# Kernel tuning notes

Measured on AMD Instinct MI355X. Metric: run time of the kernel, lower is better.

Reference implementation:

```python
import jax, jax.numpy as jnp
import numpy as np

N = 50000
E = 800000
IN_C = 16
H = 64
EA = 3
L = 3
EPS = 1e-5

def layer_norm(h, g, b):
    mu = jnp.mean(h, axis=-1, keepdims=True)
    var = jnp.var(h, axis=-1, keepdims=True)
    return (h - mu) * jax.lax.rsqrt(var + EPS) * g + b

def setup_inputs() -> dict:
    key = jax.random.key(0)
    ks = jax.random.split(key, 24)
    s = lambda *sh: 0.05
    d = {}
    d["x"] = jax.random.normal(ks[0], (N, IN_C), jnp.float32)
    d["edge_index"] = jax.random.randint(ks[1], (2, E), 0, N, jnp.int32)
    d["edge_attr"] = jax.random.normal(ks[2], (E, EA), jnp.float32)
    # encoder
    d["enc_w"] = jax.random.normal(ks[3], (IN_C, H), jnp.float32) * 0.1
    d["enc_b"] = jnp.zeros((H,), jnp.float32)
    d["enc_ln_g"] = jnp.ones((H,), jnp.float32)
    d["enc_ln_b"] = jnp.zeros((H,), jnp.float32)
    # message-passing MLPs (stacked over layers)
    d["mlp_w1"] = jax.random.normal(ks[4], (L, H + EA, H // 2), jnp.float32) * 0.1
    d["mlp_b1"] = jnp.zeros((L, H // 2), jnp.float32)
    d["mlp_w2"] = jax.random.normal(ks[5], (L, H // 2, H), jnp.float32) * 0.1
    d["mlp_b2"] = jnp.zeros((L, H), jnp.float32)
    d["ln_g"] = jnp.ones((L, H), jnp.float32)
    d["ln_b"] = jnp.zeros((L, H), jnp.float32)
    # heads
    d["depth_w1"] = jax.random.normal(ks[6], (H, H // 2), jnp.float32) * 0.1
    d["depth_b1"] = jnp.zeros((H // 2,), jnp.float32)
    d["depth_w2"] = jax.random.normal(ks[7], (H // 2, 1), jnp.float32) * 0.1
    d["depth_b2"] = jnp.zeros((1,), jnp.float32)
    d["vel_w1"] = jax.random.normal(ks[8], (H, H // 2), jnp.float32) * 0.1
    d["vel_b1"] = jnp.zeros((H // 2,), jnp.float32)
    d["vel_w2"] = jax.random.normal(ks[9], (H // 2, 2), jnp.float32) * 0.1
    d["vel_b2"] = jnp.zeros((2,), jnp.float32)
    return d

def reference(x, edge_index, edge_attr, enc_w, enc_b, enc_ln_g, enc_ln_b,
              mlp_w1, mlp_b1, mlp_w2, mlp_b2, ln_g, ln_b,
              depth_w1, depth_b1, depth_w2, depth_b2,
              vel_w1, vel_b1, vel_w2, vel_b2):
    src, dst = edge_index[0], edge_index[1]  # PyG: x_j = x[src], aggregate at dst
    # encoder (dropout inactive in eval mode)
    h = layer_norm(x @ enc_w + enc_b, enc_ln_g, enc_ln_b)
    h = jax.nn.relu(h)
    # in-degree counts for mean aggregation (isolated nodes -> 0, like PyG)
    cnt = jax.ops.segment_sum(jnp.ones((E,), jnp.float32), dst, num_segments=N)
    inv_cnt = jnp.where(cnt > 0, 1.0 / jnp.maximum(cnt, 1.0), 0.0)[:, None]
    for i in range(L):
        m_in = jnp.concatenate([h[src], edge_attr], axis=1)          # [E, H+EA]
        m = jax.nn.relu(m_in @ mlp_w1[i] + mlp_b1[i]) @ mlp_w2[i] + mlp_b2[i]  # [E, H]
        agg = jax.ops.segment_sum(m, dst, num_segments=N) * inv_cnt  # mean aggregate
        h = layer_norm(h + agg, ln_g[i], ln_b[i])
    depth = jax.nn.relu(h @ depth_w1 + depth_b1) @ depth_w2 + depth_b2    # [N,1]
    velocity = jax.nn.relu(h @ vel_w1 + vel_b1) @ vel_w2 + vel_b2         # [N,2]
    return (depth, velocity)
```

## Files before the change

### kernel.cpp

```cpp
#include <hip/hip_runtime.h>
#include <hip/hip_bf16.h>
#include <hip/hip_fp16.h>

typedef __hip_bfloat16 bf16;
typedef unsigned int u32;
typedef unsigned int u2v __attribute__((ext_vector_type(2)));

#define NN 50000
#define NE 800000
#define INC 16
#define HD 64
#define EPSV 1e-5f
#define NB1 196
#define CNTB 3125
#define ENCB 12500

__device__ __forceinline__ float b2f(bf16 v) { return __bfloat162float(v); }
__device__ __forceinline__ bool is_bf(const void* det) {
  return *(const u32*)det == 0x3F803F80u;
}

__device__ __forceinline__ uint2 ldnt2(const uint2* p) {
  u2v t = __builtin_nontemporal_load(reinterpret_cast<const u2v*>(p));
  uint2 r; r.x = t[0]; r.y = t[1];
  return r;
}

template<typename T> __device__ __forceinline__ float ldv(const T* p, int i);
template<> __device__ __forceinline__ float ldv<float>(const float* p, int i) { return p[i]; }
template<> __device__ __forceinline__ float ldv<bf16>(const bf16* p, int i) { return b2f(p[i]); }

#define W1F   0
#define B1F   6432
#define W2F   6528
#define B2F   12672
#define DW1F  12864
#define DB1F  14912
#define DW2F  14944
#define DB2F  14976
#define VW1F  14977
#define VB1F  17025
#define VW2F  17057
#define VB2F  17121
#define WFTOT 17123

#define H_OFF    0
#define P0_OFF   3200000
#define CSR_OFF  4800000
#define WF_OFF   8000000
#define CNTI_OFF (WF_OFF + WFTOT)
#define RS_OFF   (CNTI_OFF + NN)
#define BSUM_OFF (RS_OFF + NN)
#define BOFF_OFF (BSUM_OFF + 256)
#define LPOS_OFF (BOFF_OFF + 256)
#define INV_OFF  (LPOS_OFF + NE)
#define P1_OFF   (INV_OFF + NE)
#define WS_NEED_ROOMY ((size_t)(P1_OFF + NN * 16) * 4)

template<typename T>
__device__ __forceinline__ void prep_body(
    const T* w1, const T* b1, const T* w2, const T* b2,
    const T* dw1, const T* db1, const T* dw2, const T* db2,
    const T* vw1, const T* vb1, const T* vw2, const T* vb2,
    float* wf, int i) {
  float v;
  if      (i < B1F)  v = ldv(w1,  i - W1F);
  else if (i < W2F)  v = ldv(b1,  i - B1F);
  else if (i < B2F)  v = ldv(w2,  i - W2F);
  else if (i < DW1F) v = ldv(b2,  i - B2F);
  else if (i < DB1F) v = ldv(dw1, i - DW1F);
  else if (i < DW2F) v = ldv(db1, i - DB1F);
  else if (i < DB2F) v = ldv(dw2, i - DW2F);
  else if (i < VW1F) v = ldv(db2, i - DB2F);
  else if (i < VB1F) v = ldv(vw1, i - VW1F);
  else if (i < VW2F) v = ldv(vb1, i - VB1F);
  else if (i < VB2F) v = ldv(vw2, i - VW2F);
  else               v = ldv(vb2, i - VB2F);
  wf[i] = v;
}

__global__ __launch_bounds__(256) void prep_kernel(
    const void* w1, const void* b1, const void* w2, const void* b2,
    const void* dw1, const void* db1, const void* dw2, const void* db2,
    const void* vw1, const void* vb1, const void* vw2, const void* vb2,
    float* __restrict__ wf, const void* __restrict__ det) {
  int i = blockIdx.x * blockDim.x + threadIdx.x;
  if (i >= WFTOT) return;
  if (is_bf(det))
    prep_body((const bf16*)w1, (const bf16*)b1, (const bf16*)w2, (const bf16*)b2,
              (const bf16*)dw1, (const bf16*)db1, (const bf16*)dw2, (const bf16*)db2,
              (const bf16*)vw1, (const bf16*)vb1, (const bf16*)vw2, (const bf16*)vb2, wf, i);
  else
    prep_body((const float*)w1, (const float*)b1, (const float*)w2, (const float*)b2,
              (const float*)dw1, (const float*)db1, (const float*)dw2, (const float*)db2,
              (const float*)vw1, (const float*)vb1, (const float*)vw2, (const float*)vb2, wf, i);
}

__global__ __launch_bounds__(256) void enc_count_kernel(
    const void* __restrict__ x, const void* __restrict__ enc_w,
    const void* __restrict__ enc_b, const void* __restrict__ g,
    const void* __restrict__ b, float* __restrict__ h,
    __half* __restrict__ pout, const float* __restrict__ nw1,
    const float* __restrict__ nb1, const int* __restrict__ ei,
    int* __restrict__ cnt, int* __restrict__ lpos,
    const void* __restrict__ det) {
  if (blockIdx.x < CNTB) {
    int e = blockIdx.x * 256 + threadIdx.x;
    if (e < NE) lpos[e] = atomicAdd(&cnt[ei[NE + e]], 1);
    return;
  }
  __shared__ float shv[4][64];
  int node = ((blockIdx.x - CNTB) * blockDim.x + threadIdx.x) >> 6;
  int lane = threadIdx.x & 63;
  int w = threadIdx.x >> 6;
  if (node >= NN) return;
  int jl = lane & 31, half = lane >> 5;
  float xv[INC], wv[INC], ebv, gv, bv;
  if (is_bf(det)) {
    const bf16* xp = (const bf16*)x + node * INC;
    const bf16* wp = (const bf16*)enc_w;
    #pragma unroll
    for (int k = 0; k < INC; k++) { xv[k] = b2f(xp[k]); wv[k] = b2f(wp[k * HD + lane]); }
    ebv = b2f(((const bf16*)enc_b)[lane]);
    gv  = b2f(((const bf16*)g)[lane]);
    bv  = b2f(((const bf16*)b)[lane]);
  } else {
    const float* xp = (const float*)x + node * INC;
    const float* wp = (const float*)enc_w;
    #pragma unroll
    for (int k = 0; k < INC; k++) { xv[k] = xp[k]; wv[k] = wp[k * HD + lane]; }
    ebv = ((const float*)enc_b)[lane];
    gv  = ((const float*)g)[lane];
    bv  = ((const float*)b)[lane];
  }
  float acc = ebv;
  #pragma unroll
  for (int k = 0; k < INC; k++) acc += xv[k] * wv[k];
  float s1 = acc, s2 = acc * acc;
  #pragma unroll
  for (int o = 32; o; o >>= 1) { s1 += __shfl_xor(s1, o); s2 += __shfl_xor(s2, o); }
  float mu = s1 * (1.0f / 64.0f);
  float var = fmaxf(s2 * (1.0f / 64.0f) - mu * mu, 0.0f);
  float d = acc - mu;
  float hv = fmaxf(d * rsqrtf(var + EPSV) * gv + bv, 0.0f);
  h[node * HD + lane] = hv;
  shv[w][lane] = hv;
  float pacc = 0.0f;
  int kb = half << 5;
  #pragma unroll
  for (int k4 = 0; k4 < 32; k4 += 4) {
    float4 h4 = *reinterpret_cast<const float4*>(&shv[w][kb + k4]);
    int kk = kb + k4;
    pacc += h4.x * nw1[kk * 32 + jl] + h4.y * nw1[(kk + 1) * 32 + jl]
          + h4.z * nw1[(kk + 2) * 32 + jl] + h4.w * nw1[(kk + 3) * 32 + jl];
  }
  pacc += __shfl_xor(pacc, 32);
  if (half == 0) pout[node * 32 + jl] = __float2half(pacc + nb1[jl]);
}

__global__ __launch_bounds__(256) void scan1_kernel(const int* __restrict__ cnt,
                                                    int* __restrict__ ex,
                                                    int* __restrict__ bsum) {
  __shared__ int s[256];
  int t = threadIdx.x, idx = blockIdx.x * 256 + t;
  int v = (idx < NN) ? cnt[idx] : 0;
  s[t] = v;
  __syncthreads();
  #pragma unroll
  for (int off = 1; off < 256; off <<= 1) {
    int u = (t >= off) ? s[t - off] : 0;
    __syncthreads();
    s[t] += u;
    __syncthreads();
  }
  if (idx < NN) ex[idx] = s[t] - v;
  if (t == 255) bsum[blockIdx.x] = s[255];
}

__global__ __launch_bounds__(256) void scan2_kernel(int* __restrict__ bsum,
                                                    int* __restrict__ boff) {
  __shared__ int s[256];
  int t = threadIdx.x;
  int v = (t < NB1) ? bsum[t] : 0;
  s[t] = v;
  __syncthreads();
  #pragma unroll
  for (int off = 1; off < 256; off <<= 1) {
    int u = (t >= off) ? s[t - off] : 0;
    __syncthreads();
    s[t] += u;
    __syncthreads();
  }
  boff[t] = s[t] - v;
}

__global__ __launch_bounds__(256) void scan3_kernel(int* __restrict__ rs,
                                                    const int* __restrict__ boff) {
  int idx = blockIdx.x * 256 + threadIdx.x;
  if (idx >= NN) return;
  rs[idx] += boff[blockIdx.x];
}

__global__ __launch_bounds__(256) void inv_kernel(const int* __restrict__ ei,
                                                  const int* __restrict__ rs,
                                                  const int* __restrict__ lpos,
                                                  int* __restrict__ inv) {
  int e = blockIdx.x * blockDim.x + threadIdx.x;
  if (e >= NE) return;
  int dst = ei[NE + e];
  inv[rs[dst] + lpos[e]] = e;
}

__global__ __launch_bounds__(256) void fill_kernel(const int* __restrict__ inv,
                                                   const int* __restrict__ ei,
                                                   const void* __restrict__ attr,
                                                   uint2* __restrict__ csr,
                                                   const void* __restrict__ det) {
  int p = blockIdx.x * blockDim.x + threadIdx.x;
  if (p >= NE) return;
  int e = inv[p];
  u32 src = (u32)ei[e];
  float a0, a1, a2;
  if (is_bf(det)) {
    const bf16* ap = (const bf16*)attr + 3 * e;
    a0 = b2f(ap[0]); a1 = b2f(ap[1]); a2 = b2f(ap[2]);
  } else {
    const float* ap = (const float*)attr + 3 * e;
    a0 = ap[0]; a1 = ap[1]; a2 = ap[2];
  }
  u32 lo = ((u32)__half_as_ushort(__float2half(a1)) << 16)
         | (u32)__half_as_ushort(__float2half(a0));
  u32 hi = (src << 16) | (u32)__half_as_ushort(__float2half(a2));
  uint2 v; v.x = lo; v.y = hi;
  csr[p] = v;
}

__global__ __launch_bounds__(256) void node_pre_kernel(
    const float* __restrict__ h, const float* __restrict__ w1,
    const float* __restrict__ b1, __half* __restrict__ p) {
  int t = blockIdx.x * blockDim.x + threadIdx.x;
  int node = t >> 5;
  int j = t & 31;
  if (node >= NN) return;
  const float* hr = h + node * HD;
  float acc = b1[j];
  #pragma unroll
  for (int k = 0; k < HD; k++) acc += hr[k] * w1[k * 32 + j];
  p[node * 32 + j] = __float2half(acc);
}

__global__ __launch_bounds__(128) void gather_kernel(
    float* __restrict__ h, const __half2* __restrict__ pin,
    __half* __restrict__ pnext, const uint2* __restrict__ csr,
    const int* __restrict__ rs, const int* __restrict__ cnt,
    const float* __restrict__ w1a, const float* __restrict__ w2,
    const float* __restrict__ b2v, const void* __restrict__ gbase,
    const void* __restrict__ bbase, int layer,
    const float* __restrict__ nw1, const float* __restrict__ nb1,
    int do_pnext, const float* __restrict__ wf, void* __restrict__ out,
    const void* __restrict__ det) {
  __shared__ float sacc[2][2][32];
  __shared__ float shv[2][2][64];
  int wid = (blockIdx.x * blockDim.x + threadIdx.x) >> 6;
  int lane = threadIdx.x & 63;
  int w = threadIdx.x >> 6;
  int n0 = 2 * wid, n1 = 2 * wid + 1;
  if (n0 >= NN) return;
  int jl = lane & 31, half = lane >> 5;
  int q4 = lane >> 4, pp = lane & 15;
  float2 wa0 = *reinterpret_cast<const float2*>(&w1a[2 * pp]);
  float2 wa1 = *reinterpret_cast<const float2*>(&w1a[32 + 2 * pp]);
  float2 wa2 = *reinterpret_cast<const float2*>(&w1a[64 + 2 * pp]);
  int s0 = rs[n0], c0 = cnt[n0];
  int s1 = rs[n1], c1 = cnt[n1];
  float hres0 = h[n0 * HD + lane];
  float hres1 = h[n1 * HD + lane];
  float b2l = b2v[lane];

  bool isbf = is_bf(det);
  int gidx = layer * HD + lane;
  float gv, bv;
  if (isbf) {
    gv = b2f(((const bf16*)gbase)[gidx]);
    bv = b2f(((const bf16*)bbase)[gidx]);
  } else {
    gv = ((const float*)gbase)[gidx];
    bv = ((const float*)bbase)[gidx];
  }

  int cm10 = (c0 > 0) ? c0 - 1 : 0;
  int cm11 = (c1 > 0) ? c1 - 1 : 0;
  int t0 = (c0 > 0) ? s0 : 0;
  int t1 = (c1 > 0) ? s1 : 0;

  float2 acc0 = make_float2(0.f, 0.f), acc1 = make_float2(0.f, 0.f);
  int cmax = max(c0, c1);
  if (cmax > 0) {
    uint2 e0[4], e1[4];
    #pragma unroll
    for (int t = 0; t < 4; t++) {
      e0[t] = ldnt2(&csr[t0 + min(4 * t + q4, cm10)]);
      e1[t] = ldnt2(&csr[t1 + min(4 * t + q4, cm11)]);
    }
    for (int b0 = 0; b0 < cmax; b0 += 16) {
      float2 g0[4], g1[4];
      #pragma unroll
      for (int t = 0; t < 4; t++)
        g0[t] = __half22float2(pin[(e0[t].y >> 16) * 16 + pp]);
      #pragma unroll
      for (int t = 0; t < 4; t++)
        g1[t] = __half22float2(pin[(e1[t].y >> 16) * 16 + pp]);
      float2 pa0[4], pa1[4];
      #pragma unroll
      for (int t = 0; t < 4; t++) {
        float2 a01 = __half22float2(*reinterpret_cast<const __half2*>(&e0[t].x));
        float a2 = __half2float(__ushort_as_half((unsigned short)(e0[t].y & 0xFFFFu)));
        pa0[t].x = a01.x * wa0.x + a01.y * wa1.x + a2 * wa2.x;
        pa0[t].y = a01.x * wa0.y + a01.y * wa1.y + a2 * wa2.y;
        float2 b01 = __half22float2(*reinterpret_cast<const __half2*>(&e1[t].x));
        float b2 = __half2float(__ushort_as_half((unsigned short)(e1[t].y & 0xFFFFu)));
        pa1[t].x = b01.x * wa0.x + b01.y * wa1.x + b2 * wa2.x;
        pa1[t].y = b01.x * wa0.y + b01.y * wa1.y + b2 * wa2.y;
      }
      int nb = b0 + 16;
      if (nb < cmax) {
        #pragma unroll
        for (int t = 0; t < 4; t++) {
          e0[t] = ldnt2(&csr[t0 + min(nb + 4 * t + q4, cm10)]);
          e1[t] = ldnt2(&csr[t1 + min(nb + 4 * t + q4, cm11)]);
        }
      }
      #pragma unroll
      for (int t = 0; t < 4; t++) {
        int eo = b0 + 4 * t + q4;
        float rx0 = fmaxf(g0[t].x + pa0[t].x, 0.0f);
        float ry0 = fmaxf(g0[t].y + pa0[t].y, 0.0f);
        acc0.x += (eo < c0) ? rx0 : 0.0f;
        acc0.y += (eo < c0) ? ry0 : 0.0f;
        float rx1 = fmaxf(g1[t].x + pa1[t].x, 0.0f);
        float ry1 = fmaxf(g1[t].y + pa1[t].y, 0.0f);
        acc1.x += (eo < c1) ? rx1 : 0.0f;
        acc1.y += (eo < c1) ? ry1 : 0.0f;
      }
    }
  }
  acc0.x += __shfl_xor(acc0.x, 16); acc0.y += __shfl_xor(acc0.y, 16);
  acc1.x += __shfl_xor(acc1.x, 16); acc1.y += __shfl_xor(acc1.y, 16);
  acc0.x += __shfl_xor(acc0.x, 32); acc0.y += __shfl_xor(acc0.y, 32);
  acc1.x += __shfl_xor(acc1.x, 32); acc1.y += __shfl_xor(acc1.y, 32);
  if (lane < 16) {
    *reinterpret_cast<float2*>(&sacc[w][0][2 * pp]) = acc0;
    *reinterpret_cast<float2*>(&sacc[w][1][2 * pp]) = acc1;
  }

  float m0 = 0.0f, m1 = 0.0f;
  #pragma unroll
  for (int j4 = 0; j4 < 32; j4 += 4) {
    float4 a0 = *reinterpret_cast<const float4*>(&sacc[w][0][j4]);
    float4 a1 = *reinterpret_cast<const float4*>(&sacc[w][1][j4]);
    float w20 = w2[(j4 + 0) * HD + lane], w21 = w2[(j4 + 1) * HD + lane];
    float w22 = w2[(j4 + 2) * HD + lane], w23 = w2[(j4 + 3) * HD + lane];
    m0 += a0.x * w20 + a0.y * w21 + a0.z * w22 + a0.w * w23;
    m1 += a1.x * w20 + a1.y * w21 + a1.z * w22 + a1.w * w23;
  }
  float aggv0 = (c0 > 0) ? (m0 / (float)c0 + b2l) : 0.0f;
  float aggv1 = (c1 > 0) ? (m1 / (float)c1 + b2l) : 0.0f;

  float v0 = hres0 + aggv0, v1 = hres1 + aggv1;
  float s10 = v0, s20 = v0 * v0, s11 = v1, s21 = v1 * v1;
  #pragma unroll
  for (int o = 32; o; o >>= 1) {
    s10 += __shfl_xor(s10, o); s20 += __shfl_xor(s20, o);
    s11 += __shfl_xor(s11, o); s21 += __shfl_xor(s21, o);
  }
  float mu0 = s10 * (1.0f / 64.0f), mu1 = s11 * (1.0f / 64.0f);
  float var0 = fmaxf(s20 * (1.0f / 64.0f) - mu0 * mu0, 0.0f);
  float var1 = fmaxf(s21 * (1.0f / 64.0f) - mu1 * mu1, 0.0f);
  float hv0 = (v0 - mu0) * rsqrtf(var0 + EPSV) * gv + bv;
  float hv1 = (v1 - mu1) * rsqrtf(var1 + EPSV) * gv + bv;

  shv[w][0][lane] = hv0;
  shv[w][1][lane] = hv1;

  if (do_pnext) {
    float p0a = 0.0f, p1a = 0.0f;
    int kb = half << 5;
    #pragma unroll
    for (int k4 = 0; k4 < 32; k4 += 4) {
      float4 h0 = *reinterpret_cast<const float4*>(&shv[w][0][kb + k4]);
      float4 h1 = *reinterpret_cast<const float4*>(&shv[w][1][kb + k4]);
      int kk = kb + k4;
      float n0v = nw1[kk * 32 + jl], n1v = nw1[(kk + 1) * 32 + jl];
      float n2v = nw1[(kk + 2) * 32 + jl], n3v = nw1[(kk + 3) * 32 + jl];
      p0a += h0.x * n0v + h0.y * n1v + h0.z * n2v + h0.w * n3v;
      p1a += h1.x * n0v + h1.y * n1v + h1.z * n2v + h1.w * n3v;
    }
    p0a += __shfl_xor(p0a, 32);
    p1a += __shfl_xor(p1a, 32);
    if (half == 0) {
      pnext[n0 * 32 + jl] = __float2half(p0a + nb1[jl]);
      pnext[n1 * 32 + jl] = __float2half(p1a + nb1[jl]);
    }
  }

  if (layer == 2) {
    const float* w1h = wf + (half ? VW1F : DW1F);
    float a20 = half ? wf[VB1F + jl] : wf[DB1F + jl];
    float a21 = a20;
    #pragma unroll
    for (int k4 = 0; k4 < 64; k4 += 4) {
      float4 h0 = *reinterpret_cast<const float4*>(&shv[w][0][k4]);
      float4 h1 = *reinterpret_cast<const float4*>(&shv[w][1][k4]);
      float wv0 = w1h[(k4 + 0) * 32 + jl], wv1 = w1h[(k4 + 1) * 32 + jl];
      float wv2 = w1h[(k4 + 2) * 32 + jl], wv3 = w1h[(k4 + 3) * 32 + jl];
      a20 += h0.x * wv0 + h0.y * wv1 + h0.z * wv2 + h0.w * wv3;
      a21 += h1.x * wv0 + h1.y * wv1 + h1.z * wv2 + h1.w * wv3;
    }
    a20 = fmaxf(a20, 0.0f);
    a21 = fmaxf(a21, 0.0f);
    float r00, r10, r01, r11;
    if (half == 0) {
      r00 = a20 * wf[DW2F + jl]; r10 = 0.0f;
      r01 = a21 * wf[DW2F + jl]; r11 = 0.0f;
    } else {
      r00 = a20 * wf[VW2F + 2 * jl]; r10 = a20 * wf[VW2F + 2 * jl + 1];
      r01 = a21 * wf[VW2F + 2 * jl]; r11 = a21 * wf[VW2F + 2 * jl + 1];
    }
    #pragma unroll
    for (int o = 16; o; o >>= 1) {
      r00 += __shfl_xor(r00, o); r10 += __shfl_xor(r10, o);
      r01 += __shfl_xor(r01, o); r11 += __shfl_xor(r11, o);
    }
    if (lane == 0) {
      float d0 = r00 + wf[DB2F];
      float d1 = r01 + wf[DB2F];
      if (isbf) {
        ((bf16*)out)[n0] = __float2bfloat16(d0);
        ((bf16*)out)[n1] = __float2bfloat16(d1);
      } else {
        ((float*)out)[n0] = d0;
        ((float*)out)[n1] = d1;
      }
    }
    if (lane == 32) {
      float v00 = r00 + wf[VB2F], v01 = r10 + wf[VB2F + 1];
      float v10 = r01 + wf[VB2F], v11 = r11 + wf[VB2F + 1];
      if (isbf) {
        ((bf16*)out)[NN + 2 * n0]     = __float2bfloat16(v00);
        ((bf16*)out)[NN + 2 * n0 + 1] = __float2bfloat16(v01);
        ((bf16*)out)[NN + 2 * n1]     = __float2bfloat16(v10);
        ((bf16*)out)[NN + 2 * n1 + 1] = __float2bfloat16(v11);
      } else {
        ((float*)out)[NN + 2 * n0]     = v00;
        ((float*)out)[NN + 2 * n0 + 1] = v01;
        ((float*)out)[NN + 2 * n1]     = v10;
        ((float*)out)[NN + 2 * n1 + 1] = v11;
      }
    }
  } else {
    h[n0 * HD + lane] = hv0;
    h[n1 * HD + lane] = hv1;
  }
}

extern "C" void kernel_launch(void* const* d_in, const int* in_sizes, int n_in,
                              void* d_out, int out_size, void* d_ws, size_t ws_size,
                              hipStream_t stream) {
  const void* x     = d_in[0];
  const int*  ei    = (const int*)d_in[1];
  const void* attr  = d_in[2];
  const void* enc_w = d_in[3];
  const void* enc_b = d_in[4];
  const void* enc_g = d_in[5];
  const void* enc_bb= d_in[6];
  const void* mw1   = d_in[7];
  const void* mb1   = d_in[8];
  const void* mw2   = d_in[9];
  const void* mb2   = d_in[10];
  const void* lng   = d_in[11];
  const void* lnb   = d_in[12];
  const void* dw1   = d_in[13];
  const void* db1   = d_in[14];
  const void* dw2   = d_in[15];
  const void* db2   = d_in[16];
  const void* vw1   = d_in[17];
  const void* vb1   = d_in[18];
  const void* vw2   = d_in[19];
  const void* vb2   = d_in[20];

  float* ws    = (float*)d_ws;
  float* h     = ws + H_OFF;
  __half* p0   = (__half*)(ws + P0_OFF);
  uint2* csr   = (uint2*)(ws + CSR_OFF);
  float* wf    = ws + WF_OFF;
  int*   cnti  = (int*)(ws + CNTI_OFF);
  int*   rs    = (int*)(ws + RS_OFF);
  int*   bsum  = (int*)(ws + BSUM_OFF);
  int*   boff  = (int*)(ws + BOFF_OFF);
  int*   lpos  = (int*)(ws + LPOS_OFF);
  int*   inv   = (int*)(ws + INV_OFF);
  __half* p1   = (__half*)(ws + P1_OFF);
  bool roomy = ws_size >= WS_NEED_ROOMY;

  hipMemsetAsync(cnti, 0, (size_t)NN * sizeof(int), stream);
  prep_kernel<<<(WFTOT + 255) / 256, 256, 0, stream>>>(
      mw1, mb1, mw2, mb2, dw1, db1, dw2, db2, vw1, vb1, vw2, vb2, wf, enc_g);
  enc_count_kernel<<<CNTB + ENCB, 256, 0, stream>>>(
      x, enc_w, enc_b, enc_g, enc_bb, h, p0, wf + W1F, wf + B1F,
      ei, cnti, lpos, enc_g);
  scan1_kernel<<<NB1, 256, 0, stream>>>(cnti, rs, bsum);
  scan2_kernel<<<1, 256, 0, stream>>>(bsum, boff);
  scan3_kernel<<<NB1, 256, 0, stream>>>(rs, boff);
  inv_kernel<<<(NE + 255) / 256, 256, 0, stream>>>(ei, rs, lpos, inv);
  fill_kernel<<<(NE + 255) / 256, 256, 0, stream>>>(inv, ei, attr, csr, enc_g);

  for (int l = 0; l < 3; l++) {
    __half* pin  = (roomy && (l & 1)) ? p1 : p0;
    __half* pnxt = (roomy && !(l & 1)) ? p1 : p0;
    if (!roomy && l > 0) {
      node_pre_kernel<<<(NN * 32 + 255) / 256, 256, 0, stream>>>(
          h, wf + W1F + l * 2144, wf + B1F + l * 32, p0);
      pin = p0; pnxt = p0;
    }
    int do_pnext = (roomy && l < 2) ? 1 : 0;
    int nl = (l < 2) ? l + 1 : l;
    gather_kernel<<<(NN + 3) / 4, 128, 0, stream>>>(
        h, (const __half2*)pin, pnxt, csr, rs, cnti,
        wf + W1F + l * 2144 + 64 * 32, wf + W2F + l * 2048, wf + B2F + l * 64,
        lng, lnb, l,
        wf + W1F + nl * 2144, wf + B1F + nl * 32, do_pnext,
        wf, d_out, enc_g);
  }
}
```

Measured before the change: 340.8 us.

## Drop lpos array and scan3 pass; encode two nodes per wave

The counting pass no longer stores each edge's atomic return slot. inv_kernel instead takes a second atomic counter per destination, and the block offset from the scan is added on the fly, both in inv_kernel and in gather_kernel, which removes the scan3 launch. The encoder now processes two nodes per wavefront and launches half as many blocks, so weight loads are amortised. The cost is an extra atomic pass and a larger memset. Edge order inside each CSR segment becomes nondeterministic, which can slightly change float summation order.

```diff
diff --git a/kernel.cpp b/kernel.cpp
--- a/kernel.cpp
+++ b/kernel.cpp
@@ -13,7 +13,7 @@
 #define EPSV 1e-5f
 #define NB1 196
 #define CNTB 3125
-#define ENCB 12500
+#define ENCB 6250
 
 __device__ __forceinline__ float b2f(bf16 v) { return __bfloat162float(v); }
 __device__ __forceinline__ bool is_bf(const void* det) {
@@ -49,11 +49,11 @@
 #define CSR_OFF  4800000
 #define WF_OFF   8000000
 #define CNTI_OFF (WF_OFF + WFTOT)
-#define RS_OFF   (CNTI_OFF + NN)
+#define CNT2_OFF (CNTI_OFF + NN)
+#define RS_OFF   (CNT2_OFF + NN)
 #define BSUM_OFF (RS_OFF + NN)
 #define BOFF_OFF (BSUM_OFF + 256)
-#define LPOS_OFF (BOFF_OFF + 256)
-#define INV_OFF  (LPOS_OFF + NE)
+#define INV_OFF  (BOFF_OFF + 256)
 #define P1_OFF   (INV_OFF + NE)
 #define WS_NEED_ROOMY ((size_t)(P1_OFF + NN * 16) * 4)
 
@@ -102,60 +102,79 @@
     const void* __restrict__ b, float* __restrict__ h,
     __half* __restrict__ pout, const float* __restrict__ nw1,
     const float* __restrict__ nb1, const int* __restrict__ ei,
-    int* __restrict__ cnt, int* __restrict__ lpos,
-    const void* __restrict__ det) {
+    int* __restrict__ cnt, const void* __restrict__ det) {
   if (blockIdx.x < CNTB) {
     int e = blockIdx.x * 256 + threadIdx.x;
-    if (e < NE) lpos[e] = atomicAdd(&cnt[ei[NE + e]], 1);
+    if (e < NE) atomicAdd(&cnt[ei[NE + e]], 1);
     return;
   }
-  __shared__ float shv[4][64];
-  int node = ((blockIdx.x - CNTB) * blockDim.x + threadIdx.x) >> 6;
+  __shared__ float shv[4][2][64];
+  int wid = ((blockIdx.x - CNTB) * blockDim.x + threadIdx.x) >> 6;
   int lane = threadIdx.x & 63;
   int w = threadIdx.x >> 6;
-  if (node >= NN) return;
+  int n0 = 2 * wid, n1 = n0 + 1;
+  if (n0 >= NN) return;
   int jl = lane & 31, half = lane >> 5;
-  float xv[INC], wv[INC], ebv, gv, bv;
+  float xv0[INC], xv1[INC], wv[INC], ebv, gv, bv;
   if (is_bf(det)) {
-    const bf16* xp = (const bf16*)x + node * INC;
+    const bf16* xp0 = (const bf16*)x + n0 * INC;
+    const bf16* xp1 = (const bf16*)x + n1 * INC;
     const bf16* wp = (const bf16*)enc_w;
     #pragma unroll
-    for (int k = 0; k < INC; k++) { xv[k] = b2f(xp[k]); wv[k] = b2f(wp[k * HD + lane]); }
+    for (int k = 0; k < INC; k++) {
+      xv0[k] = b2f(xp0[k]); xv1[k] = b2f(xp1[k]); wv[k] = b2f(wp[k * HD + lane]);
+    }
     ebv = b2f(((const bf16*)enc_b)[lane]);
     gv  = b2f(((const bf16*)g)[lane]);
     bv  = b2f(((const bf16*)b)[lane]);
   } else {
-    const float* xp = (const float*)x + node * INC;
+    const float* xp0 = (const float*)x + n0 * INC;
+    const float* xp1 = (const float*)x + n1 * INC;
     const float* wp = (const float*)enc_w;
     #pragma unroll
-    for (int k = 0; k < INC; k++) { xv[k] = xp[k]; wv[k] = wp[k * HD + lane]; }
+    for (int k = 0; k < INC; k++) {
+      xv0[k] = xp0[k]; xv1[k] = xp1[k]; wv[k] = wp[k * HD + lane];
+    }
     ebv = ((const float*)enc_b)[lane];
     gv  = ((const float*)g)[lane];
     bv  = ((const float*)b)[lane];
   }
-  float acc = ebv;
-  #pragma unroll
-  for (int k = 0; k < INC; k++) acc += xv[k] * wv[k];
-  float s1 = acc, s2 = acc * acc;
-  #pragma unroll
-  for (int o = 32; o; o >>= 1) { s1 += __shfl_xor(s1, o); s2 += __shfl_xor(s2, o); }
-  float mu = s1 * (1.0f / 64.0f);
-  float var = fmaxf(s2 * (1.0f / 64.0f) - mu * mu, 0.0f);
-  float d = acc - mu;
-  float hv = fmaxf(d * rsqrtf(var + EPSV) * gv + bv, 0.0f);
-  h[node * HD + lane] = hv;
-  shv[w][lane] = hv;
-  float pacc = 0.0f;
+  float acc0 = ebv, acc1 = ebv;
+  #pragma unroll
+  for (int k = 0; k < INC; k++) { acc0 += xv0[k] * wv[k]; acc1 += xv1[k] * wv[k]; }
+  float s10 = acc0, s20 = acc0 * acc0, s11 = acc1, s21 = acc1 * acc1;
+  #pragma unroll
+  for (int o = 32; o; o >>= 1) {
+    s10 += __shfl_xor(s10, o); s20 += __shfl_xor(s20, o);
+    s11 += __shfl_xor(s11, o); s21 += __shfl_xor(s21, o);
+  }
+  float mu0 = s10 * (1.0f / 64.0f), mu1 = s11 * (1.0f / 64.0f);
+  float var0 = fmaxf(s20 * (1.0f / 64.0f) - mu0 * mu0, 0.0f);
+  float var1 = fmaxf(s21 * (1.0f / 64.0f) - mu1 * mu1, 0.0f);
+  float hv0 = fmaxf((acc0 - mu0) * rsqrtf(var0 + EPSV) * gv + bv, 0.0f);
+  float hv1 = fmaxf((acc1 - mu1) * rsqrtf(var1 + EPSV) * gv + bv, 0.0f);
+  h[n0 * HD + lane] = hv0;
+  h[n1 * HD + lane] = hv1;
+  shv[w][0][lane] = hv0;
+  shv[w][1][lane] = hv1;
+  float pacc0 = 0.0f, pacc1 = 0.0f;
   int kb = half << 5;
   #pragma unroll
   for (int k4 = 0; k4 < 32; k4 += 4) {
-    float4 h4 = *reinterpret_cast<const float4*>(&shv[w][kb + k4]);
+    float4 h0 = *reinterpret_cast<const float4*>(&shv[w][0][kb + k4]);
+    float4 h1 = *reinterpret_cast<const float4*>(&shv[w][1][kb + k4]);
     int kk = kb + k4;
-    pacc += h4.x * nw1[kk * 32 + jl] + h4.y * nw1[(kk + 1) * 32 + jl]
-          + h4.z * nw1[(kk + 2) * 32 + jl] + h4.w * nw1[(kk + 3) * 32 + jl];
-  }
-  pacc += __shfl_xor(pacc, 32);
-  if (half == 0) pout[node * 32 + jl] = __float2half(pacc + nb1[jl]);
+    float n0v = nw1[kk * 32 + jl],       n1v = nw1[(kk + 1) * 32 + jl];
+    float n2v = nw1[(kk + 2) * 32 + jl], n3v = nw1[(kk + 3) * 32 + jl];
+    pacc0 += h0.x * n0v + h0.y * n1v + h0.z * n2v + h0.w * n3v;
+    pacc1 += h1.x * n0v + h1.y * n1v + h1.z * n2v + h1.w * n3v;
+  }
+  pacc0 += __shfl_xor(pacc0, 32);
+  pacc1 += __shfl_xor(pacc1, 32);
+  if (half == 0) {
+    pout[n0 * 32 + jl] = __float2half(pacc0 + nb1[jl]);
+    pout[n1 * 32 + jl] = __float2half(pacc1 + nb1[jl]);
+  }
 }
 
 __global__ __launch_bounds__(256) void scan1_kernel(const int* __restrict__ cnt,
@@ -194,21 +213,16 @@
   boff[t] = s[t] - v;
 }
 
-__global__ __launch_bounds__(256) void scan3_kernel(int* __restrict__ rs,
-                                                    const int* __restrict__ boff) {
-  int idx = blockIdx.x * 256 + threadIdx.x;
-  if (idx >= NN) return;
-  rs[idx] += boff[blockIdx.x];
-}
-
 __global__ __launch_bounds__(256) void inv_kernel(const int* __restrict__ ei,
                                                   const int* __restrict__ rs,
-                                                  const int* __restrict__ lpos,
+                                                  const int* __restrict__ boff,
+                                                  int* __restrict__ cnt2,
                                                   int* __restrict__ inv) {
   int e = blockIdx.x * blockDim.x + threadIdx.x;
   if (e >= NE) return;
   int dst = ei[NE + e];
-  inv[rs[dst] + lpos[e]] = e;
+  int pos = rs[dst] + boff[dst >> 8] + atomicAdd(&cnt2[dst], 1);
+  inv[pos] = e;
 }
 
 __global__ __launch_bounds__(256) void fill_kernel(const int* __restrict__ inv,
@@ -252,7 +266,8 @@
 __global__ __launch_bounds__(128) void gather_kernel(
     float* __restrict__ h, const __half2* __restrict__ pin,
     __half* __restrict__ pnext, const uint2* __restrict__ csr,
-    const int* __restrict__ rs, const int* __restrict__ cnt,
+    const int* __restrict__ rs, const int* __restrict__ boff,
+    const int* __restrict__ cnt,
     const float* __restrict__ w1a, const float* __restrict__ w2,
     const float* __restrict__ b2v, const void* __restrict__ gbase,
     const void* __restrict__ bbase, int layer,
@@ -271,8 +286,8 @@
   float2 wa0 = *reinterpret_cast<const float2*>(&w1a[2 * pp]);
   float2 wa1 = *reinterpret_cast<const float2*>(&w1a[32 + 2 * pp]);
   float2 wa2 = *reinterpret_cast<const float2*>(&w1a[64 + 2 * pp]);
-  int s0 = rs[n0], c0 = cnt[n0];
-  int s1 = rs[n1], c1 = cnt[n1];
+  int s0 = rs[n0] + boff[n0 >> 8], c0 = cnt[n0];
+  int s1 = rs[n1] + boff[n1 >> 8], c1 = cnt[n1];
   float hres0 = h[n0 * HD + lane];
   float hres1 = h[n1 * HD + lane];
   float b2l = b2v[lane];
@@ -494,24 +509,23 @@
   uint2* csr   = (uint2*)(ws + CSR_OFF);
   float* wf    = ws + WF_OFF;
   int*   cnti  = (int*)(ws + CNTI_OFF);
+  int*   cnt2  = (int*)(ws + CNT2_OFF);
   int*   rs    = (int*)(ws + RS_OFF);
   int*   bsum  = (int*)(ws + BSUM_OFF);
   int*   boff  = (int*)(ws + BOFF_OFF);
-  int*   lpos  = (int*)(ws + LPOS_OFF);
   int*   inv   = (int*)(ws + INV_OFF);
   __half* p1   = (__half*)(ws + P1_OFF);
   bool roomy = ws_size >= WS_NEED_ROOMY;
 
-  hipMemsetAsync(cnti, 0, (size_t)NN * sizeof(int), stream);
+  hipMemsetAsync(cnti, 0, (size_t)(2 * NN) * sizeof(int), stream);
   prep_kernel<<<(WFTOT + 255) / 256, 256, 0, stream>>>(
       mw1, mb1, mw2, mb2, dw1, db1, dw2, db2, vw1, vb1, vw2, vb2, wf, enc_g);
   enc_count_kernel<<<CNTB + ENCB, 256, 0, stream>>>(
       x, enc_w, enc_b, enc_g, enc_bb, h, p0, wf + W1F, wf + B1F,
-      ei, cnti, lpos, enc_g);
+      ei, cnti, enc_g);
   scan1_kernel<<<NB1, 256, 0, stream>>>(cnti, rs, bsum);
   scan2_kernel<<<1, 256, 0, stream>>>(bsum, boff);
-  scan3_kernel<<<NB1, 256, 0, stream>>>(rs, boff);
-  inv_kernel<<<(NE + 255) / 256, 256, 0, stream>>>(ei, rs, lpos, inv);
+  inv_kernel<<<(NE + 255) / 256, 256, 0, stream>>>(ei, rs, boff, cnt2, inv);
   fill_kernel<<<(NE + 255) / 256, 256, 0, stream>>>(inv, ei, attr, csr, enc_g);
 
   for (int l = 0; l < 3; l++) {
@@ -525,7 +539,7 @@
     int do_pnext = (roomy && l < 2) ? 1 : 0;
     int nl = (l < 2) ? l + 1 : l;
     gather_kernel<<<(NN + 3) / 4, 128, 0, stream>>>(
-        h, (const __half2*)pin, pnxt, csr, rs, cnti,
+        h, (const __half2*)pin, pnxt, csr, rs, boff, cnti,
         wf + W1F + l * 2144 + 64 * 32, wf + W2F + l * 2048, wf + B2F + l * 64,
         lng, lnb, l,
         wf + W1F + nl * 2144, wf + B1F + nl * 32, do_pnext,
```

Result: slower. 365.3 us (+7.2%).
